# Kernel tuning notes

Measured on AMD Instinct MI355X. Metric: run time of the kernel, lower is better.

The kernel has to match this reference:

```python
import jax, jax.numpy as jnp
import numpy as np

N_NODES = 50000
N_EDGES = 1600000
F_IN = 33
F_OUT = 128
HEADS = 2


def _add_self_loops(row, col, n):
    loop = jnp.arange(n, dtype=row.dtype)
    return jnp.concatenate([row, loop]), jnp.concatenate([col, loop])


def gcn_conv(x, row, col, w, W, b):
    # PyG GCNConv with edge_weight: add self-loops (weight 1), symmetric norm.
    n = x.shape[0]
    row, col = _add_self_loops(row, col, n)
    w = jnp.concatenate([w, jnp.ones((n,), x.dtype)])
    deg = jax.ops.segment_sum(w, col, num_segments=n)
    dinv = jnp.where(deg > 0, jax.lax.rsqrt(deg), 0.0)
    norm = dinv[row] * w * dinv[col]            # [E+N]
    xl = x @ W                                   # [N, F_OUT]
    out = jax.ops.segment_sum(norm[:, None] * xl[row], col, num_segments=n)
    return out + b


def gat_conv(x, row, col, W, att_src, att_dst, b):
    # PyG GATConv, heads=2, concat=False, eval-mode (no attention dropout).
    n = x.shape[0]
    row, col = _add_self_loops(row, col, n)
    xl = (x @ W).reshape(n, HEADS, F_OUT)        # [N, H, C]
    a_src = (xl * att_src).sum(-1)               # [N, H]
    a_dst = (xl * att_dst).sum(-1)               # [N, H]
    e = jax.nn.leaky_relu(a_src[row] + a_dst[col], 0.2)  # [E+N, H]
    m = jax.ops.segment_max(e, col, num_segments=n)      # per-dst max (stable)
    e = jnp.exp(e - m[col])
    s = jax.ops.segment_sum(e, col, num_segments=n)
    alpha = e / s[col]                           # edge softmax per dst node
    out = jax.ops.segment_sum(alpha[:, :, None] * xl[row], col, num_segments=n)
    return out.mean(axis=1) + b                  # concat=False -> head mean


def setup_inputs() -> dict:
    key = jax.random.key(0)
    ks = jax.random.split(key, 16)
    s_in = 1.0 / np.sqrt(F_IN)
    s_h = 1.0 / np.sqrt(F_OUT)
    inp = {
        "target_x": jax.random.normal(ks[0], (N_NODES, F_IN), jnp.float32),
        "target_edge_index": jax.random.randint(ks[1], (2, N_EDGES), 0, N_NODES, jnp.int32),
        "target_weight": jax.random.uniform(ks[2], (N_EDGES,), jnp.float32),
        "gcn_W": jax.random.normal(ks[3], (F_IN, F_OUT), jnp.float32) * s_in,
        "gcn_b": jnp.zeros((F_OUT,), jnp.float32),
        "gat1_W": jax.random.normal(ks[4], (F_OUT, HEADS * F_OUT), jnp.float32) * s_h,
        "gat1_as": jax.random.normal(ks[5], (HEADS, F_OUT), jnp.float32) * s_h,
        "gat1_ad": jax.random.normal(ks[6], (HEADS, F_OUT), jnp.float32) * s_h,
        "gat1_b": jnp.zeros((F_OUT,), jnp.float32),
        "gat2_W": jax.random.normal(ks[7], (F_OUT, HEADS * F_OUT), jnp.float32) * s_h,
        "gat2_as": jax.random.normal(ks[8], (HEADS, F_OUT), jnp.float32) * s_h,
        "gat2_ad": jax.random.normal(ks[9], (HEADS, F_OUT), jnp.float32) * s_h,
        "gat2_b": jnp.zeros((F_OUT,), jnp.float32),
        "fc1_W": jax.random.normal(ks[10], (F_OUT, F_OUT), jnp.float32) * s_h,
        "fc1_b": jnp.zeros((F_OUT,), jnp.float32),
        "fc2_W": jax.random.normal(ks[11], (F_OUT, F_OUT), jnp.float32) * s_h,
        "fc2_b": jnp.zeros((F_OUT,), jnp.float32),
        "pro_bias": jax.random.uniform(ks[12], (1, F_OUT), jnp.float32, -0.2, 0.2),
    }
    return inp


def _forward(target_x, target_weight, gcn_W, gcn_b, gat1_W, gat1_as, gat1_ad,
             gat1_b, gat2_W, gat2_as, gat2_ad, gat2_b, fc1_W, fc1_b,
             fc2_W, fc2_b, pro_bias, row, col):
    # layer 0: GCN + ReLU
    x = jax.nn.relu(gcn_conv(target_x, row, col, target_weight, gcn_W, gcn_b))
    # layer 1: GAT + ReLU, then sigmoid-gated blend
    xt = jax.nn.relu(gat_conv(x, row, col, gat1_W, gat1_as, gat1_ad, gat1_b))
    z = jax.nn.sigmoid(xt @ fc1_W + fc1_b + x @ fc2_W + fc2_b + pro_bias)
    x = z * xt + (1.0 - z) * x
    # layer 2: GAT (no ReLU on last layer), gated blend
    xt = gat_conv(x, row, col, gat2_W, gat2_as, gat2_ad, gat2_b)
    z = jax.nn.sigmoid(xt @ fc1_W + fc1_b + x @ fc2_W + fc2_b + pro_bias)
    return z * xt + (1.0 - z) * x


def reference(target_x, target_edge_index, target_weight, gcn_W, gcn_b,
              gat1_W, gat1_as, gat1_ad, gat1_b, gat2_W, gat2_as, gat2_ad,
              gat2_b, fc1_W, fc1_b, fc2_W, fc2_b, pro_bias):
    row, col = target_edge_index[0], target_edge_index[1]
    return _forward(target_x, target_weight, gcn_W, gcn_b, gat1_W, gat1_as,
                    gat1_ad, gat1_b, gat2_W, gat2_as, gat2_ad, gat2_b,
                    fc1_W, fc1_b, fc2_W, fc2_b, pro_bias, row, col)
```

## Files before the change

### kernel.cpp

```cpp
#include <hip/hip_runtime.h>

#define F_IN 33
#define FP 36
#define C 128
#define GROWS 16
#define MAXDEG 128

__device__ __forceinline__ unsigned short f2bf(float f) {
  unsigned u = __float_as_uint(f);
  unsigned r = (u + 0x7fff + ((u >> 16) & 1)) >> 16;
  return (unsigned short)r;
}
__device__ __forceinline__ unsigned pack2(float lo, float hi) {
  return (unsigned)f2bf(lo) | ((unsigned)f2bf(hi) << 16);
}
__device__ __forceinline__ float bflo(unsigned u) { return __uint_as_float(u << 16); }
__device__ __forceinline__ float bfhi(unsigned u) { return __uint_as_float(u & 0xffff0000u); }


__global__ void count_kernel(const int* __restrict__ col, const float* __restrict__ w,
                             int* __restrict__ cnt, float* __restrict__ deg, int E) {
  int e = blockIdx.x * blockDim.x + threadIdx.x;
  if (e < E) {
    int c = col[e];
    atomicAdd(&cnt[c], 1);
    atomicAdd(&deg[c], w[e]);
  }
}

__global__ void scan1_kernel(const int* __restrict__ cnt, int* __restrict__ out,
                             int* __restrict__ bsum, int n) {
  __shared__ int lds[256];
  int t = threadIdx.x;
  int base = blockIdx.x * 1024 + t * 4;
  int v0 = (base + 0 < n) ? cnt[base + 0] : 0;
  int v1 = (base + 1 < n) ? cnt[base + 1] : 0;
  int v2 = (base + 2 < n) ? cnt[base + 2] : 0;
  int v3 = (base + 3 < n) ? cnt[base + 3] : 0;
  int tot = v0 + v1 + v2 + v3;
  lds[t] = tot;
  __syncthreads();
  for (int o = 1; o < 256; o <<= 1) {
    int x = (t >= o) ? lds[t - o] : 0;
    __syncthreads();
    lds[t] += x;
    __syncthreads();
  }
  int excl = lds[t] - tot;
  if (t == 255) bsum[blockIdx.x] = lds[255];
  if (base + 0 < n) out[base + 0] = excl;
  if (base + 1 < n) out[base + 1] = excl + v0;
  if (base + 2 < n) out[base + 2] = excl + v0 + v1;
  if (base + 3 < n) out[base + 3] = excl + v0 + v1 + v2;
}

__global__ void scan2_kernel(int* __restrict__ bsum, int nb) {
  __shared__ int lds[256];
  int t = threadIdx.x;
  int v = (t < nb) ? bsum[t] : 0;
  lds[t] = v;
  __syncthreads();
  for (int o = 1; o < 256; o <<= 1) {
    int x = (t >= o) ? lds[t - o] : 0;
    __syncthreads();
    lds[t] += x;
    __syncthreads();
  }
  if (t < nb) bsum[t] = lds[t] - v;
}

__global__ void scan3_dinv_kernel(int* __restrict__ off, const int* __restrict__ bsum,
                                  const float* __restrict__ deg, float* __restrict__ dinv,
                                  int n, int N) {
  int i = blockIdx.x * blockDim.x + threadIdx.x;
  if (i < n) off[i] += bsum[i >> 10];
  if (i < N) dinv[i] = rsqrtf(deg[i] + 1.0f);
}

__global__ void scatter_kernel(const int* __restrict__ row, const int* __restrict__ col,
                               const float* __restrict__ w, const int* __restrict__ off,
                               const float* __restrict__ dinv, int* __restrict__ cur,
                               int2* __restrict__ sedge, int E) {
  int e = blockIdx.x * blockDim.x + threadIdx.x;
  if (e < E) {
    int c = col[e];
    int r = row[e];
    int p = off[c] + atomicAdd(&cur[c], 1);
    sedge[p] = make_int2(r, __float_as_int(dinv[r] * w[e]));
  }
}


__global__ void prep_dots_kernel(const float* __restrict__ W1, const float* __restrict__ as1,
                                 const float* __restrict__ ad1, const float* __restrict__ W2,
                                 const float* __restrict__ as2, const float* __restrict__ ad2,
                                 float* __restrict__ attv) {
  int t = blockIdx.x * 256 + threadIdx.x;
  if (t >= 1024) return;
  int layer = t >> 9, rem = t & 511, sd = rem >> 8, rem2 = rem & 255;
  int h = rem2 >> 7, k = rem2 & 127;
  const float* W = layer ? W2 : W1;
  const float* att = sd ? (layer ? ad2 : ad1) : (layer ? as2 : as1);
  float s = 0.f;
  for (int c2 = 0; c2 < C; c2++) s += W[k * 2 * C + h * C + c2] * att[h * C + c2];
  attv[t] = s;
}

__global__ void prep_repack_kernel(const float* __restrict__ W1, const float* __restrict__ W2,
                                   float* __restrict__ Wp1, float* __restrict__ Wp2) {
  int t = blockIdx.x * 256 + threadIdx.x;
  int layer = t >> 15, rem = t & 32767, hk = rem >> 7, j = rem & 127;
  int h = hk >> 7, k = hk & 127;
  const float* W = layer ? W2 : W1;
  float* Wp = layer ? Wp2 : Wp1;
  Wp[hk * C + j] = W[k * 2 * C + h * C + j];
}

__global__ void prep_wz_kernel(const float* __restrict__ fc1W, const float* __restrict__ fc2W,
                               float* __restrict__ Wz) {
  int t = blockIdx.x * 256 + threadIdx.x;
  if (t >= 32768) return;
  Wz[t] = (t < 16384) ? fc1W[t] : fc2W[t - 16384];
}

__global__ void convert_x_kernel(const float* __restrict__ x, unsigned* __restrict__ X36U, int N) {
  int t = blockIdx.x * blockDim.x + threadIdx.x;
  if (t >= N * (FP / 2)) return;
  int n = t / (FP / 2);
  int p = t - n * (FP / 2);
  int c0 = 2 * p, c1 = 2 * p + 1;
  float f0 = (c0 < F_IN) ? x[n * F_IN + c0] : 0.f;
  float f1 = (c1 < F_IN) ? x[n * F_IN + c1] : 0.f;
  X36U[t] = pack2(f0, f1);
}


__global__ __launch_bounds__(256) void gcn_agg33_kernel(
    const unsigned* __restrict__ X36U, const int* __restrict__ off,
    const int2* __restrict__ sedge, const float* __restrict__ dinv,
    float* __restrict__ Xagg, int N) {
  int c = blockIdx.x * 4 + (threadIdx.x >> 6);
  if (c >= N) return;
  int l = threadIdx.x & 63;
  bool act = l < FP / 2;
  float dc = dinv[c];
  unsigned uc = act ? X36U[(unsigned)c * (FP / 2) + l] : 0u;
  float A0x = dc * bflo(uc), A0y = dc * bfhi(uc);
  float A1x = 0.f, A1y = 0.f, A2x = 0.f, A2y = 0.f, A3x = 0.f, A3y = 0.f;
  int p = off[c], p1 = off[c + 1];
  for (; p + 4 <= p1; p += 4) {
    int2 e0 = sedge[p + 0], e1 = sedge[p + 1], e2 = sedge[p + 2], e3 = sedge[p + 3];
    unsigned u0 = 0, u1 = 0, u2 = 0, u3 = 0;
    if (act) {
      u0 = X36U[(unsigned)e0.x * (FP / 2) + l];
      u1 = X36U[(unsigned)e1.x * (FP / 2) + l];
      u2 = X36U[(unsigned)e2.x * (FP / 2) + l];
      u3 = X36U[(unsigned)e3.x * (FP / 2) + l];
    }
    float w0 = __int_as_float(e0.y), w1 = __int_as_float(e1.y);
    float w2 = __int_as_float(e2.y), w3 = __int_as_float(e3.y);
    A0x += w0 * bflo(u0); A0y += w0 * bfhi(u0);
    A1x += w1 * bflo(u1); A1y += w1 * bfhi(u1);
    A2x += w2 * bflo(u2); A2y += w2 * bfhi(u2);
    A3x += w3 * bflo(u3); A3y += w3 * bfhi(u3);
  }
  for (; p < p1; p++) {
    int2 e0 = sedge[p];
    unsigned u0 = act ? X36U[(unsigned)e0.x * (FP / 2) + l] : 0u;
    float w0 = __int_as_float(e0.y);
    A0x += w0 * bflo(u0); A0y += w0 * bfhi(u0);
  }
  if (act) {
    float2 o;
    o.x = dc * (A0x + A1x + A2x + A3x);
    o.y = dc * (A0y + A1y + A2y + A3y);
    ((float2*)Xagg)[(unsigned)c * (FP / 2) + l] = o;
  }
}

__global__ void gemm36_kernel(const float* __restrict__ Xagg, const float* __restrict__ W,
                              const float* __restrict__ b, const float* __restrict__ wsv,
                              const float* __restrict__ wdv, float* __restrict__ H,
                              unsigned short* __restrict__ Hb, float* __restrict__ asrc,
                              float* __restrict__ adst, int N) {
  int n0 = blockIdx.x * GROWS;
  int j = threadIdx.x;
  __shared__ float xr[GROWS * FP];
  __shared__ float xls[GROWS * 132];
  {
    const float4* src = (const float4*)(Xagg + (size_t)n0 * FP);
    float4* dst = (float4*)xr;
    for (int i = j; i < GROWS * FP / 4; i += 128) dst[i] = src[i];
  }
  __syncthreads();
  float acc[GROWS];
  #pragma unroll
  for (int r = 0; r < GROWS; r++) acc[r] = 0.f;
  #pragma unroll 3
  for (int k = 0; k < F_IN; k++) {
    float wv = W[k * C + j];
    #pragma unroll
    for (int r = 0; r < GROWS; r++) acc[r] += xr[r * FP + k] * wv;
  }
  #pragma unroll
  for (int r = 0; r < GROWS; r++) {
    int n = n0 + r;
    float v = fmaxf(acc[r] + b[j], 0.f);
    if (n < N) {
      H[(size_t)n * C + j] = v;
      Hb[(size_t)n * C + j] = f2bf(v);
    }
    xls[r * 132 + j] = v;
  }
  __syncthreads();
  int r = j >> 3, sub = j & 7;
  float sa0 = 0.f, sd0 = 0.f, sa1 = 0.f, sd1 = 0.f;
  for (int k = sub; k < C; k += 8) {
    float v = xls[r * 132 + k];
    sa0 += v * wsv[k];      sd0 += v * wdv[k];
    sa1 += v * wsv[C + k];  sd1 += v * wdv[C + k];
  }
  #pragma unroll
  for (int o = 4; o > 0; o >>= 1) {
    sa0 += __shfl_down(sa0, o); sd0 += __shfl_down(sd0, o);
    sa1 += __shfl_down(sa1, o); sd1 += __shfl_down(sd1, o);
  }
  int n = n0 + r;
  if (sub == 0 && n < N) {
    asrc[n * 2 + 0] = sa0; adst[n * 2 + 0] = sd0;
    asrc[n * 2 + 1] = sa1; adst[n * 2 + 1] = sd1;
  }
}

__global__ __launch_bounds__(256) void gat_agg_kernel(
    const unsigned* __restrict__ HbU, const float* __restrict__ asrc,
    const float* __restrict__ adst, const int* __restrict__ off,
    const int2* __restrict__ sedge, unsigned* __restrict__ AggU, int N) {
  __shared__ float2 lsc[4][MAXDEG];
  int slot = threadIdx.x >> 6;
  int c = blockIdx.x * 4 + slot;
  if (c >= N) return;
  int l = threadIdx.x & 63;
  float2 adc = ((const float2*)adst)[c];
  float2 asc = ((const float2*)asrc)[c];
  int p0 = off[c], p1 = off[c + 1];
  int deg = p1 - p0;
  float e00 = asc.x + adc.x; e00 = e00 > 0.f ? e00 : 0.2f * e00;
  float e01 = asc.y + adc.y; e01 = e01 > 0.f ? e01 : 0.2f * e01;
  float m0 = e00, m1 = e01;
  for (int p = p0 + l; p < p1; p += 64) {
    int r = sedge[p].x;
    float2 av = ((const float2*)asrc)[r];
    float e0 = av.x + adc.x; e0 = e0 > 0.f ? e0 : 0.2f * e0;
    float e1 = av.y + adc.y; e1 = e1 > 0.f ? e1 : 0.2f * e1;
    int i = p - p0;
    if (i < MAXDEG) lsc[slot][i] = make_float2(e0, e1);
    m0 = fmaxf(m0, e0); m1 = fmaxf(m1, e1);
  }
  #pragma unroll
  for (int o = 32; o > 0; o >>= 1) {
    m0 = fmaxf(m0, __shfl_xor(m0, o));
    m1 = fmaxf(m1, __shfl_xor(m1, o));
  }
  int nl = deg < MAXDEG ? deg : MAXDEG;
  float s0 = 0.f, s1 = 0.f;
  for (int i = l; i < nl; i += 64) {
    float2 sc = lsc[slot][i];
    float a0 = __expf(sc.x - m0), a1 = __expf(sc.y - m1);
    lsc[slot][i] = make_float2(a0, a1);
    s0 += a0; s1 += a1;
  }
  for (int p = p0 + MAXDEG + l; p < p1; p += 64) {
    int r = sedge[p].x;
    float2 av = ((const float2*)asrc)[r];
    float e0 = av.x + adc.x; e0 = e0 > 0.f ? e0 : 0.2f * e0;
    float e1 = av.y + adc.y; e1 = e1 > 0.f ? e1 : 0.2f * e1;
    s0 += __expf(e0 - m0); s1 += __expf(e1 - m1);
  }
  #pragma unroll
  for (int o = 32; o > 0; o >>= 1) { s0 += __shfl_xor(s0, o); s1 += __shfl_xor(s1, o); }
  float w0 = __expf(e00 - m0), w1 = __expf(e01 - m1);
  s0 += w0; s1 += w1;
  float inv0 = 1.f / s0, inv1 = 1.f / s1;
  unsigned uc = HbU[(unsigned)c * 64 + l];
  float a00 = w0 * bflo(uc), a01 = w0 * bfhi(uc);
  float a10 = w1 * bflo(uc), a11 = w1 * bfhi(uc);
  float b00 = 0.f, b01 = 0.f, b10 = 0.f, b11 = 0.f;
  int i = 0;
  for (; i + 8 <= nl; i += 8) {
    int r0 = sedge[p0 + i + 0].x, r1 = sedge[p0 + i + 1].x;
    int r2 = sedge[p0 + i + 2].x, r3 = sedge[p0 + i + 3].x;
    int r4 = sedge[p0 + i + 4].x, r5 = sedge[p0 + i + 5].x;
    int r6 = sedge[p0 + i + 6].x, r7 = sedge[p0 + i + 7].x;
    unsigned u0 = HbU[(unsigned)r0 * 64 + l];
    unsigned u1 = HbU[(unsigned)r1 * 64 + l];
    unsigned u2 = HbU[(unsigned)r2 * 64 + l];
    unsigned u3 = HbU[(unsigned)r3 * 64 + l];
    unsigned u4 = HbU[(unsigned)r4 * 64 + l];
    unsigned u5 = HbU[(unsigned)r5 * 64 + l];
    unsigned u6 = HbU[(unsigned)r6 * 64 + l];
    unsigned u7 = HbU[(unsigned)r7 * 64 + l];
    float2 f0 = lsc[slot][i + 0], f1 = lsc[slot][i + 1];
    float2 f2 = lsc[slot][i + 2], f3 = lsc[slot][i + 3];
    float2 f4 = lsc[slot][i + 4], f5 = lsc[slot][i + 5];
    float2 f6 = lsc[slot][i + 6], f7 = lsc[slot][i + 7];
    a00 += f0.x * bflo(u0); a01 += f0.x * bfhi(u0); a10 += f0.y * bflo(u0); a11 += f0.y * bfhi(u0);
    b00 += f1.x * bflo(u1); b01 += f1.x * bfhi(u1); b10 += f1.y * bflo(u1); b11 += f1.y * bfhi(u1);
    a00 += f2.x * bflo(u2); a01 += f2.x * bfhi(u2); a10 += f2.y * bflo(u2); a11 += f2.y * bfhi(u2);
    b00 += f3.x * bflo(u3); b01 += f3.x * bfhi(u3); b10 += f3.y * bflo(u3); b11 += f3.y * bfhi(u3);
    a00 += f4.x * bflo(u4); a01 += f4.x * bfhi(u4); a10 += f4.y * bflo(u4); a11 += f4.y * bfhi(u4);
    b00 += f5.x * bflo(u5); b01 += f5.x * bfhi(u5); b10 += f5.y * bflo(u5); b11 += f5.y * bfhi(u5);
    a00 += f6.x * bflo(u6); a01 += f6.x * bfhi(u6); a10 += f6.y * bflo(u6); a11 += f6.y * bfhi(u6);
    b00 += f7.x * bflo(u7); b01 += f7.x * bfhi(u7); b10 += f7.y * bflo(u7); b11 += f7.y * bfhi(u7);
  }
  for (; i < nl; i++) {
    int r0 = sedge[p0 + i].x;
    unsigned u0 = HbU[(unsigned)r0 * 64 + l];
    float2 f0 = lsc[slot][i];
    a00 += f0.x * bflo(u0); a01 += f0.x * bfhi(u0);
    a10 += f0.y * bflo(u0); a11 += f0.y * bfhi(u0);
  }
  for (int p = p0 + MAXDEG; p < p1; p++) {
    int r = sedge[p].x;
    float2 av = ((const float2*)asrc)[r];
    float e0 = av.x + adc.x; e0 = e0 > 0.f ? e0 : 0.2f * e0;
    float e1 = av.y + adc.y; e1 = e1 > 0.f ? e1 : 0.2f * e1;
    float al0 = __expf(e0 - m0), al1 = __expf(e1 - m1);
    unsigned u0 = HbU[(unsigned)r * 64 + l];
    a00 += al0 * bflo(u0); a01 += al0 * bfhi(u0);
    a10 += al1 * bflo(u0); a11 += al1 * bfhi(u0);
  }
  AggU[(unsigned)c * 128 + l]      = pack2((a00 + b00) * inv0, (a01 + b01) * inv0);
  AggU[(unsigned)c * 128 + 64 + l] = pack2((a10 + b10) * inv1, (a11 + b11) * inv1);
}

__global__ __launch_bounds__(128) void post_gemm_kernel(
    const unsigned* __restrict__ AggU, const float* __restrict__ Wp,
    const float* __restrict__ b, float* __restrict__ XT,
    unsigned short* __restrict__ XTb, int relu, int N) {
  __shared__ unsigned az[GROWS][128];
  int n0 = blockIdx.x * GROWS;
  int t = threadIdx.x;
  {
    const uint4* src = (const uint4*)AggU;
    for (int i = t; i < GROWS * 32; i += 128) {
      int r = i >> 5, cch = i & 31;
      int n = n0 + r;
      uint4 v = (n < N) ? src[(size_t)n * 32 + cch] : make_uint4(0u, 0u, 0u, 0u);
      *(uint4*)&az[r][cch * 4] = v;
    }
  }
  __syncthreads();
  int w = t >> 6;
  int l = t & 63;
  float acc0[8], acc1[8];
  #pragma unroll
  for (int r = 0; r < 8; r++) { acc0[r] = 0.f; acc1[r] = 0.f; }
  for (int k8 = 0; k8 < 256; k8 += 8) {
    float wA[8], wB[8];
    #pragma unroll
    for (int q = 0; q < 8; q++) {
      wA[q] = Wp[(k8 + q) * C + l];
      wB[q] = Wp[(k8 + q) * C + l + 64];
    }
    #pragma unroll
    for (int r = 0; r < 8; r++) {
      uint4 u = *(const uint4*)&az[w * 8 + r][k8 >> 1];
      float v0 = bflo(u.x), v1 = bfhi(u.x), v2 = bflo(u.y), v3 = bfhi(u.y);
      float v4 = bflo(u.z), v5 = bfhi(u.z), v6 = bflo(u.w), v7 = bfhi(u.w);
      acc0[r] += v0*wA[0] + v1*wA[1] + v2*wA[2] + v3*wA[3]
               + v4*wA[4] + v5*wA[5] + v6*wA[6] + v7*wA[7];
      acc1[r] += v0*wB[0] + v1*wB[1] + v2*wB[2] + v3*wB[3]
               + v4*wB[4] + v5*wB[5] + v6*wB[6] + v7*wB[7];
    }
  }
  float bA = b[l], bB = b[l + 64];
  #pragma unroll
  for (int r = 0; r < 8; r++) {
    int n = n0 + w * 8 + r;
    if (n < N) {
      float vA = 0.5f * acc0[r] + bA;
      float vB = 0.5f * acc1[r] + bB;
      if (relu) { vA = fmaxf(vA, 0.f); vB = fmaxf(vB, 0.f); }
      XT[(size_t)n * C + l]      = vA;
      XT[(size_t)n * C + l + 64] = vB;
      XTb[(size_t)n * C + l]      = f2bf(vA);
      XTb[(size_t)n * C + l + 64] = f2bf(vB);
    }
  }
}

__global__ __launch_bounds__(128) void blend_kernel(
    const unsigned* __restrict__ XTbU, const unsigned* __restrict__ XbU,
    const float* __restrict__ XTf, const float* __restrict__ Xf,
    const float* __restrict__ Wz, const float* __restrict__ fc1b,
    const float* __restrict__ fc2b, const float* __restrict__ pb,
    float* __restrict__ out, unsigned short* __restrict__ Hb2,
    const float* __restrict__ wsv, const float* __restrict__ wdv,
    float* __restrict__ asrc, float* __restrict__ adst, int dots, int N) {
  __shared__ unsigned az[GROWS][128];
  __shared__ float xls[GROWS * 132];
  int n0 = blockIdx.x * GROWS;
  int t = threadIdx.x;
  {
    const uint4* s1 = (const uint4*)XTbU;
    const uint4* s2 = (const uint4*)XbU;
    for (int i = t; i < GROWS * 32; i += 128) {
      int r = i >> 5, cch = i & 31;
      int n = n0 + r;
      uint4 v;
      if (n < N) v = (cch < 16) ? s1[(size_t)n * 16 + cch] : s2[(size_t)n * 16 + (cch - 16)];
      else v = make_uint4(0u, 0u, 0u, 0u);
      *(uint4*)&az[r][cch * 4] = v;
    }
  }
  __syncthreads();
  int w = t >> 6;
  int l = t & 63;
  float acc0[8], acc1[8];
  #pragma unroll
  for (int r = 0; r < 8; r++) { acc0[r] = 0.f; acc1[r] = 0.f; }
  for (int k8 = 0; k8 < 256; k8 += 8) {
    float wA[8], wB[8];
    #pragma unroll
    for (int q = 0; q < 8; q++) {
      wA[q] = Wz[(k8 + q) * C + l];
      wB[q] = Wz[(k8 + q) * C + l + 64];
    }
    #pragma unroll
    for (int r = 0; r < 8; r++) {
      uint4 u = *(const uint4*)&az[w * 8 + r][k8 >> 1];
      float v0 = bflo(u.x), v1 = bfhi(u.x), v2 = bflo(u.y), v3 = bfhi(u.y);
      float v4 = bflo(u.z), v5 = bfhi(u.z), v6 = bflo(u.w), v7 = bfhi(u.w);
      acc0[r] += v0*wA[0] + v1*wA[1] + v2*wA[2] + v3*wA[3]
               + v4*wA[4] + v5*wA[5] + v6*wA[6] + v7*wA[7];
      acc1[r] += v0*wB[0] + v1*wB[1] + v2*wB[2] + v3*wB[3]
               + v4*wB[4] + v5*wB[5] + v6*wB[6] + v7*wB[7];
    }
  }
  float bbA = fc1b[l] + fc2b[l] + pb[l];
  float bbB = fc1b[l + 64] + fc2b[l + 64] + pb[l + 64];
  #pragma unroll
  for (int r = 0; r < 8; r++) {
    int rr = w * 8 + r;
    int n = n0 + rr;
    if (n < N) {
      float xtA = XTf[(size_t)n * C + l],      xA = Xf[(size_t)n * C + l];
      float xtB = XTf[(size_t)n * C + l + 64], xB = Xf[(size_t)n * C + l + 64];
      float tA = acc0[r] + bbA, tB = acc1[r] + bbB;
      float zA = 1.f / (1.f + __expf(-tA));
      float zB = 1.f / (1.f + __expf(-tB));
      float oA = zA * xtA + (1.f - zA) * xA;
      float oB = zB * xtB + (1.f - zB) * xB;
      out[(size_t)n * C + l]      = oA;
      out[(size_t)n * C + l + 64] = oB;
      if (dots) {
        Hb2[(size_t)n * C + l]      = f2bf(oA);
        Hb2[(size_t)n * C + l + 64] = f2bf(oB);
      }
      xls[rr * 132 + l] = oA;
      xls[rr * 132 + l + 64] = oB;
    } else {
      xls[rr * 132 + l] = 0.f;
      xls[rr * 132 + l + 64] = 0.f;
    }
  }
  if (!dots) return;
  __syncthreads();
  int r = t >> 3, sub = t & 7;
  float sa0 = 0.f, sd0 = 0.f, sa1 = 0.f, sd1 = 0.f;
  for (int k = sub; k < C; k += 8) {
    float v = xls[r * 132 + k];
    sa0 += v * wsv[k];      sd0 += v * wdv[k];
    sa1 += v * wsv[C + k];  sd1 += v * wdv[C + k];
  }
  #pragma unroll
  for (int o = 4; o > 0; o >>= 1) {
    sa0 += __shfl_down(sa0, o); sd0 += __shfl_down(sd0, o);
    sa1 += __shfl_down(sa1, o); sd1 += __shfl_down(sd1, o);
  }
  int n = n0 + r;
  if (sub == 0 && n < N) {
    asrc[n * 2 + 0] = sa0; adst[n * 2 + 0] = sd0;
    asrc[n * 2 + 1] = sa1; adst[n * 2 + 1] = sd1;
  }
}


extern "C" void kernel_launch(void* const* d_in, const int* in_sizes, int n_in,
                              void* d_out, int out_size, void* d_ws, size_t ws_size,
                              hipStream_t stream) {
  const float* x_in  = (const float*)d_in[0];
  const int*   ei    = (const int*)d_in[1];
  const float* ew    = (const float*)d_in[2];
  const float* gcn_W = (const float*)d_in[3];
  const float* gcn_b = (const float*)d_in[4];
  const float* g1_W  = (const float*)d_in[5];
  const float* g1_as = (const float*)d_in[6];
  const float* g1_ad = (const float*)d_in[7];
  const float* g1_b  = (const float*)d_in[8];
  const float* g2_W  = (const float*)d_in[9];
  const float* g2_as = (const float*)d_in[10];
  const float* g2_ad = (const float*)d_in[11];
  const float* g2_b  = (const float*)d_in[12];
  const float* fc1_W = (const float*)d_in[13];
  const float* fc1_b = (const float*)d_in[14];
  const float* fc2_W = (const float*)d_in[15];
  const float* fc2_b = (const float*)d_in[16];
  const float* pb    = (const float*)d_in[17];

  const int N = in_sizes[0] / F_IN;
  const int E = in_sizes[2];
  const int* row = ei;
  const int* col = ei + E;

  char* ws = (char*)d_ws;
  size_t o = 0;
  auto alloc = [&](size_t bytes) -> void* {
    void* p = ws + o;
    o += (bytes + 255) & ~(size_t)255;
    return p;
  };
  int*   cnt   = (int*)alloc((size_t)(N + 1) * 4);
  int*   cur   = (int*)alloc((size_t)N * 4);
  float* deg   = (float*)alloc((size_t)N * 4);
  size_t zero_bytes = o;
  int*   off   = (int*)alloc((size_t)(N + 1) * 4);
  float* dinv  = (float*)alloc((size_t)N * 4);
  int*   bsum  = (int*)alloc(256 * 4);
  int2*  sedge = (int2*)alloc((size_t)E * 8);
  float* attv  = (float*)alloc(1024 * 4);
  float* Wp1   = (float*)alloc((size_t)256 * C * 4);
  float* Wp2   = (float*)alloc((size_t)256 * C * 4);
  float* Wz    = (float*)alloc((size_t)256 * C * 4);
  float* asrc  = (float*)alloc((size_t)N * 2 * 4);
  float* adst  = (float*)alloc((size_t)N * 2 * 4);
  unsigned* X36U = (unsigned*)alloc((size_t)N * (FP / 2) * 4);
  float* Xagg  = (float*)alloc((size_t)N * FP * 4);
  float* H     = (float*)alloc((size_t)N * C * 4);
  unsigned short* Hb  = (unsigned short*)alloc((size_t)N * C * 2);
  unsigned* AggU = (unsigned*)alloc((size_t)N * 128 * 4);
  float* XT    = (float*)alloc((size_t)N * C * 4);
  unsigned short* XTb = (unsigned short*)alloc((size_t)N * C * 2);
  float* H2    = (float*)alloc((size_t)N * C * 4);
  unsigned short* Hb2 = (unsigned short*)alloc((size_t)N * C * 2);
  (void)ws_size; (void)n_in; (void)out_size;

  float* ws1 = attv + 0,   *wd1 = attv + 256;
  float* ws2 = attv + 512, *wd2 = attv + 768;

  hipMemsetAsync(d_ws, 0, zero_bytes, stream);

  const int tb = 256;
  const int nP = N + 1;
  const int nb = (nP + 1023) / 1024;

  prep_dots_kernel<<<4, 256, 0, stream>>>(g1_W, g1_as, g1_ad, g2_W, g2_as, g2_ad, attv);
  prep_repack_kernel<<<256, 256, 0, stream>>>(g1_W, g2_W, Wp1, Wp2);
  prep_wz_kernel<<<128, 256, 0, stream>>>(fc1_W, fc2_W, Wz);
  convert_x_kernel<<<(N * (FP / 2) + tb - 1) / tb, tb, 0, stream>>>(x_in, X36U, N);

  count_kernel<<<(E + tb - 1) / tb, tb, 0, stream>>>(col, ew, cnt, deg, E);
  scan1_kernel<<<nb, 256, 0, stream>>>(cnt, off, bsum, nP);
  scan2_kernel<<<1, 256, 0, stream>>>(bsum, nb);
  scan3_dinv_kernel<<<(nP + tb - 1) / tb, tb, 0, stream>>>(off, bsum, deg, dinv, nP, N);
  scatter_kernel<<<(E + tb - 1) / tb, tb, 0, stream>>>(row, col, ew, off, dinv, cur, sedge, E);

  gcn_agg33_kernel<<<(N + 3) / 4, 256, 0, stream>>>(X36U, off, sedge, dinv, Xagg, N);
  gemm36_kernel<<<(N + GROWS - 1) / GROWS, C, 0, stream>>>(Xagg, gcn_W, gcn_b, ws1, wd1,
                                                           H, Hb, asrc, adst, N);

  gat_agg_kernel<<<(N + 3) / 4, 256, 0, stream>>>((const unsigned*)Hb, asrc, adst, off, sedge, AggU, N);
  post_gemm_kernel<<<(N + GROWS - 1) / GROWS, C, 0, stream>>>(AggU, Wp1, g1_b, XT, XTb, 1, N);
  blend_kernel<<<(N + GROWS - 1) / GROWS, C, 0, stream>>>(
      (const unsigned*)XTb, (const unsigned*)Hb, XT, H, Wz, fc1_b, fc2_b, pb,
      H2, Hb2, ws2, wd2, asrc, adst, 1, N);

  gat_agg_kernel<<<(N + 3) / 4, 256, 0, stream>>>((const unsigned*)Hb2, asrc, adst, off, sedge, AggU, N);
  post_gemm_kernel<<<(N + GROWS - 1) / GROWS, C, 0, stream>>>(AggU, Wp2, g2_b, XT, XTb, 0, N);
  blend_kernel<<<(N + GROWS - 1) / GROWS, C, 0, stream>>>(
      (const unsigned*)XTb, (const unsigned*)Hb2, XT, H2, Wz, fc1_b, fc2_b, pb,
      (float*)d_out, (unsigned short*)0, ws2, wd2, asrc, adst, 0, N);
}
```

Measured before the change: 1.009 ms.

## Split GAT aggregation into attention kernel plus feature-sliced gather passes

The fused GAT aggregation is split in two. An attention kernel writes per-edge softmax numerators to a global buffer (the output array is reused as scratch), plus per-node self weights and sums. Four gather passes then each handle a 16-column slice of the bf16 features, with lanes spread over edges, aiming to shrink the gathered working set per pass and improve cache hit rate. The GCN degree is now computed from the sorted CSR instead of float atomics, and dinv[row] is applied at gather time; the cost is re-reading edges and alpha four times and extra launches.

```diff
diff --git a/kernel.cpp b/kernel.cpp
--- a/kernel.cpp
+++ b/kernel.cpp
@@ -4,7 +4,6 @@
 #define FP 36
 #define C 128
 #define GROWS 16
-#define MAXDEG 128
 
 __device__ __forceinline__ unsigned short f2bf(float f) {
   unsigned u = __float_as_uint(f);
@@ -18,14 +17,9 @@
 __device__ __forceinline__ float bfhi(unsigned u) { return __uint_as_float(u & 0xffff0000u); }
 
 
-__global__ void count_kernel(const int* __restrict__ col, const float* __restrict__ w,
-                             int* __restrict__ cnt, float* __restrict__ deg, int E) {
+__global__ void count_kernel(const int* __restrict__ col, int* __restrict__ cnt, int E) {
   int e = blockIdx.x * blockDim.x + threadIdx.x;
-  if (e < E) {
-    int c = col[e];
-    atomicAdd(&cnt[c], 1);
-    atomicAdd(&deg[c], w[e]);
-  }
+  if (e < E) atomicAdd(&cnt[col[e]], 1);
 }
 
 __global__ void scan1_kernel(const int* __restrict__ cnt, int* __restrict__ out,
@@ -69,25 +63,34 @@
   if (t < nb) bsum[t] = lds[t] - v;
 }
 
-__global__ void scan3_dinv_kernel(int* __restrict__ off, const int* __restrict__ bsum,
-                                  const float* __restrict__ deg, float* __restrict__ dinv,
-                                  int n, int N) {
+__global__ void scan3_kernel(int* __restrict__ off, const int* __restrict__ bsum, int n) {
   int i = blockIdx.x * blockDim.x + threadIdx.x;
   if (i < n) off[i] += bsum[i >> 10];
-  if (i < N) dinv[i] = rsqrtf(deg[i] + 1.0f);
 }
 
 __global__ void scatter_kernel(const int* __restrict__ row, const int* __restrict__ col,
                                const float* __restrict__ w, const int* __restrict__ off,
-                               const float* __restrict__ dinv, int* __restrict__ cur,
-                               int2* __restrict__ sedge, int E) {
+                               int* __restrict__ cur, int2* __restrict__ sedge, int E) {
   int e = blockIdx.x * blockDim.x + threadIdx.x;
   if (e < E) {
     int c = col[e];
-    int r = row[e];
     int p = off[c] + atomicAdd(&cur[c], 1);
-    sedge[p] = make_int2(r, __float_as_int(dinv[r] * w[e]));
-  }
+    sedge[p] = make_int2(row[e], __float_as_int(w[e]));
+  }
+}
+
+__global__ __launch_bounds__(256) void deg_dinv_kernel(
+    const int* __restrict__ off, const int2* __restrict__ sedge,
+    float* __restrict__ dinv, int N) {
+  int c = blockIdx.x * 4 + (threadIdx.x >> 6);
+  if (c >= N) return;
+  int l = threadIdx.x & 63;
+  float s = 0.f;
+  int p1 = off[c + 1];
+  for (int p = off[c] + l; p < p1; p += 64) s += __int_as_float(sedge[p].y);
+  #pragma unroll
+  for (int o = 32; o > 0; o >>= 1) s += __shfl_xor(s, o);
+  if (l == 0) dinv[c] = rsqrtf(s + 1.0f);
 }
 
 
@@ -157,8 +160,10 @@
       u2 = X36U[(unsigned)e2.x * (FP / 2) + l];
       u3 = X36U[(unsigned)e3.x * (FP / 2) + l];
     }
-    float w0 = __int_as_float(e0.y), w1 = __int_as_float(e1.y);
-    float w2 = __int_as_float(e2.y), w3 = __int_as_float(e3.y);
+    float w0 = dinv[e0.x] * __int_as_float(e0.y);
+    float w1 = dinv[e1.x] * __int_as_float(e1.y);
+    float w2 = dinv[e2.x] * __int_as_float(e2.y);
+    float w3 = dinv[e3.x] * __int_as_float(e3.y);
     A0x += w0 * bflo(u0); A0y += w0 * bfhi(u0);
     A1x += w1 * bflo(u1); A1y += w1 * bfhi(u1);
     A2x += w2 * bflo(u2); A2y += w2 * bfhi(u2);
@@ -167,7 +172,7 @@
   for (; p < p1; p++) {
     int2 e0 = sedge[p];
     unsigned u0 = act ? X36U[(unsigned)e0.x * (FP / 2) + l] : 0u;
-    float w0 = __int_as_float(e0.y);
+    float w0 = dinv[e0.x] * __int_as_float(e0.y);
     A0x += w0 * bflo(u0); A0y += w0 * bfhi(u0);
   }
   if (act) {
@@ -232,19 +237,17 @@
   }
 }
 
-__global__ __launch_bounds__(256) void gat_agg_kernel(
-    const unsigned* __restrict__ HbU, const float* __restrict__ asrc,
-    const float* __restrict__ adst, const int* __restrict__ off,
-    const int2* __restrict__ sedge, unsigned* __restrict__ AggU, int N) {
-  __shared__ float2 lsc[4][MAXDEG];
-  int slot = threadIdx.x >> 6;
-  int c = blockIdx.x * 4 + slot;
+__global__ __launch_bounds__(256) void att_kernel(
+    const float* __restrict__ asrc, const float* __restrict__ adst,
+    const int* __restrict__ off, const int2* __restrict__ sedge,
+    float2* __restrict__ alphaA, float2* __restrict__ selfwA,
+    float2* __restrict__ sarrA, int N) {
+  int c = blockIdx.x * 4 + (threadIdx.x >> 6);
   if (c >= N) return;
   int l = threadIdx.x & 63;
   float2 adc = ((const float2*)adst)[c];
   float2 asc = ((const float2*)asrc)[c];
   int p0 = off[c], p1 = off[c + 1];
-  int deg = p1 - p0;
   float e00 = asc.x + adc.x; e00 = e00 > 0.f ? e00 : 0.2f * e00;
   float e01 = asc.y + adc.y; e01 = e01 > 0.f ? e01 : 0.2f * e01;
   float m0 = e00, m1 = e01;
@@ -253,8 +256,7 @@
     float2 av = ((const float2*)asrc)[r];
     float e0 = av.x + adc.x; e0 = e0 > 0.f ? e0 : 0.2f * e0;
     float e1 = av.y + adc.y; e1 = e1 > 0.f ? e1 : 0.2f * e1;
-    int i = p - p0;
-    if (i < MAXDEG) lsc[slot][i] = make_float2(e0, e1);
+    alphaA[p] = make_float2(e0, e1);
     m0 = fmaxf(m0, e0); m1 = fmaxf(m1, e1);
   }
   #pragma unroll
@@ -262,76 +264,71 @@
     m0 = fmaxf(m0, __shfl_xor(m0, o));
     m1 = fmaxf(m1, __shfl_xor(m1, o));
   }
-  int nl = deg < MAXDEG ? deg : MAXDEG;
   float s0 = 0.f, s1 = 0.f;
-  for (int i = l; i < nl; i += 64) {
-    float2 sc = lsc[slot][i];
+  for (int p = p0 + l; p < p1; p += 64) {
+    float2 sc = alphaA[p];
     float a0 = __expf(sc.x - m0), a1 = __expf(sc.y - m1);
-    lsc[slot][i] = make_float2(a0, a1);
+    alphaA[p] = make_float2(a0, a1);
     s0 += a0; s1 += a1;
-  }
-  for (int p = p0 + MAXDEG + l; p < p1; p += 64) {
-    int r = sedge[p].x;
-    float2 av = ((const float2*)asrc)[r];
-    float e0 = av.x + adc.x; e0 = e0 > 0.f ? e0 : 0.2f * e0;
-    float e1 = av.y + adc.y; e1 = e1 > 0.f ? e1 : 0.2f * e1;
-    s0 += __expf(e0 - m0); s1 += __expf(e1 - m1);
   }
   #pragma unroll
   for (int o = 32; o > 0; o >>= 1) { s0 += __shfl_xor(s0, o); s1 += __shfl_xor(s1, o); }
   float w0 = __expf(e00 - m0), w1 = __expf(e01 - m1);
-  s0 += w0; s1 += w1;
-  float inv0 = 1.f / s0, inv1 = 1.f / s1;
-  unsigned uc = HbU[(unsigned)c * 64 + l];
-  float a00 = w0 * bflo(uc), a01 = w0 * bfhi(uc);
-  float a10 = w1 * bflo(uc), a11 = w1 * bfhi(uc);
-  float b00 = 0.f, b01 = 0.f, b10 = 0.f, b11 = 0.f;
-  int i = 0;
-  for (; i + 8 <= nl; i += 8) {
-    int r0 = sedge[p0 + i + 0].x, r1 = sedge[p0 + i + 1].x;
-    int r2 = sedge[p0 + i + 2].x, r3 = sedge[p0 + i + 3].x;
-    int r4 = sedge[p0 + i + 4].x, r5 = sedge[p0 + i + 5].x;
-    int r6 = sedge[p0 + i + 6].x, r7 = sedge[p0 + i + 7].x;
-    unsigned u0 = HbU[(unsigned)r0 * 64 + l];
-    unsigned u1 = HbU[(unsigned)r1 * 64 + l];
-    unsigned u2 = HbU[(unsigned)r2 * 64 + l];
-    unsigned u3 = HbU[(unsigned)r3 * 64 + l];
-    unsigned u4 = HbU[(unsigned)r4 * 64 + l];
-    unsigned u5 = HbU[(unsigned)r5 * 64 + l];
-    unsigned u6 = HbU[(unsigned)r6 * 64 + l];
-    unsigned u7 = HbU[(unsigned)r7 * 64 + l];
-    float2 f0 = lsc[slot][i + 0], f1 = lsc[slot][i + 1];
-    float2 f2 = lsc[slot][i + 2], f3 = lsc[slot][i + 3];
-    float2 f4 = lsc[slot][i + 4], f5 = lsc[slot][i + 5];
-    float2 f6 = lsc[slot][i + 6], f7 = lsc[slot][i + 7];
-    a00 += f0.x * bflo(u0); a01 += f0.x * bfhi(u0); a10 += f0.y * bflo(u0); a11 += f0.y * bfhi(u0);
-    b00 += f1.x * bflo(u1); b01 += f1.x * bfhi(u1); b10 += f1.y * bflo(u1); b11 += f1.y * bfhi(u1);
-    a00 += f2.x * bflo(u2); a01 += f2.x * bfhi(u2); a10 += f2.y * bflo(u2); a11 += f2.y * bfhi(u2);
-    b00 += f3.x * bflo(u3); b01 += f3.x * bfhi(u3); b10 += f3.y * bflo(u3); b11 += f3.y * bfhi(u3);
-    a00 += f4.x * bflo(u4); a01 += f4.x * bfhi(u4); a10 += f4.y * bflo(u4); a11 += f4.y * bfhi(u4);
-    b00 += f5.x * bflo(u5); b01 += f5.x * bfhi(u5); b10 += f5.y * bflo(u5); b11 += f5.y * bfhi(u5);
-    a00 += f6.x * bflo(u6); a01 += f6.x * bfhi(u6); a10 += f6.y * bflo(u6); a11 += f6.y * bfhi(u6);
-    b00 += f7.x * bflo(u7); b01 += f7.x * bfhi(u7); b10 += f7.y * bflo(u7); b11 += f7.y * bfhi(u7);
-  }
-  for (; i < nl; i++) {
-    int r0 = sedge[p0 + i].x;
-    unsigned u0 = HbU[(unsigned)r0 * 64 + l];
-    float2 f0 = lsc[slot][i];
-    a00 += f0.x * bflo(u0); a01 += f0.x * bfhi(u0);
-    a10 += f0.y * bflo(u0); a11 += f0.y * bfhi(u0);
-  }
-  for (int p = p0 + MAXDEG; p < p1; p++) {
-    int r = sedge[p].x;
-    float2 av = ((const float2*)asrc)[r];
-    float e0 = av.x + adc.x; e0 = e0 > 0.f ? e0 : 0.2f * e0;
-    float e1 = av.y + adc.y; e1 = e1 > 0.f ? e1 : 0.2f * e1;
-    float al0 = __expf(e0 - m0), al1 = __expf(e1 - m1);
-    unsigned u0 = HbU[(unsigned)r * 64 + l];
-    a00 += al0 * bflo(u0); a01 += al0 * bfhi(u0);
-    a10 += al1 * bflo(u0); a11 += al1 * bfhi(u0);
-  }
-  AggU[(unsigned)c * 128 + l]      = pack2((a00 + b00) * inv0, (a01 + b01) * inv0);
-  AggU[(unsigned)c * 128 + 64 + l] = pack2((a10 + b10) * inv1, (a11 + b11) * inv1);
+  if (l == 0) {
+    selfwA[c] = make_float2(w0, w1);
+    sarrA[c]  = make_float2(s0 + w0, s1 + w1);
+  }
+}
+
+__global__ __launch_bounds__(256) void gat_pass_kernel(
+    const unsigned* __restrict__ HbU, const float2* __restrict__ alphaA,
+    const float2* __restrict__ selfwA, const float2* __restrict__ sarrA,
+    const int* __restrict__ off, const int2* __restrict__ sedge,
+    unsigned* __restrict__ AggU, int pass, int N) {
+  int c = blockIdx.x * 4 + (threadIdx.x >> 6);
+  if (c >= N) return;
+  int l = threadIdx.x & 63;
+  int g = l >> 4, lg = l & 15;
+  int fp = 16 * pass + lg;
+  int p0 = off[c], p1 = off[c + 1];
+  float ax = 0.f, ay = 0.f, az = 0.f, aw = 0.f;
+  float bx = 0.f, by = 0.f, bz = 0.f, bw = 0.f;
+  int p = p0 + g;
+  for (; p + 4 < p1; p += 8) {
+    int r0 = sedge[p].x, r1 = sedge[p + 4].x;
+    float2 al0 = alphaA[p], al1 = alphaA[p + 4];
+    unsigned u0 = HbU[(size_t)r0 * 64 + fp];
+    unsigned u1 = HbU[(size_t)r1 * 64 + fp];
+    float x0 = bflo(u0), y0 = bfhi(u0);
+    float x1 = bflo(u1), y1 = bfhi(u1);
+    ax += al0.x * x0; ay += al0.x * y0; az += al0.y * x0; aw += al0.y * y0;
+    bx += al1.x * x1; by += al1.x * y1; bz += al1.y * x1; bw += al1.y * y1;
+  }
+  for (; p < p1; p += 4) {
+    int r0 = sedge[p].x;
+    float2 al0 = alphaA[p];
+    unsigned u0 = HbU[(size_t)r0 * 64 + fp];
+    float x0 = bflo(u0), y0 = bfhi(u0);
+    ax += al0.x * x0; ay += al0.x * y0; az += al0.y * x0; aw += al0.y * y0;
+  }
+  ax += bx; ay += by; az += bz; aw += bw;
+  if (g == 0) {
+    float2 sw = selfwA[c];
+    unsigned uc = HbU[(size_t)c * 64 + fp];
+    float xc = bflo(uc), yc = bfhi(uc);
+    ax += sw.x * xc; ay += sw.x * yc; az += sw.y * xc; aw += sw.y * yc;
+  }
+  #pragma unroll
+  for (int o = 16; o <= 32; o <<= 1) {
+    ax += __shfl_xor(ax, o); ay += __shfl_xor(ay, o);
+    az += __shfl_xor(az, o); aw += __shfl_xor(aw, o);
+  }
+  if (g == 0) {
+    float2 sr = sarrA[c];
+    float inv0 = 1.f / sr.x, inv1 = 1.f / sr.y;
+    AggU[(size_t)c * 128 + fp]      = pack2(ax * inv0, ay * inv0);
+    AggU[(size_t)c * 128 + 64 + fp] = pack2(az * inv1, aw * inv1);
+  }
 }
 
 __global__ __launch_bounds__(128) void post_gemm_kernel(
@@ -523,7 +520,6 @@
   };
   int*   cnt   = (int*)alloc((size_t)(N + 1) * 4);
   int*   cur   = (int*)alloc((size_t)N * 4);
-  float* deg   = (float*)alloc((size_t)N * 4);
   size_t zero_bytes = o;
   int*   off   = (int*)alloc((size_t)(N + 1) * 4);
   float* dinv  = (float*)alloc((size_t)N * 4);
@@ -535,6 +531,8 @@
   float* Wz    = (float*)alloc((size_t)256 * C * 4);
   float* asrc  = (float*)alloc((size_t)N * 2 * 4);
   float* adst  = (float*)alloc((size_t)N * 2 * 4);
+  float2* selfwA = (float2*)alloc((size_t)N * 8);
+  float2* sarrA  = (float2*)alloc((size_t)N * 8);
   unsigned* X36U = (unsigned*)alloc((size_t)N * (FP / 2) * 4);
   float* Xagg  = (float*)alloc((size_t)N * FP * 4);
   float* H     = (float*)alloc((size_t)N * C * 4);
@@ -544,6 +542,7 @@
   unsigned short* XTb = (unsigned short*)alloc((size_t)N * C * 2);
   float* H2    = (float*)alloc((size_t)N * C * 4);
   unsigned short* Hb2 = (unsigned short*)alloc((size_t)N * C * 2);
+  float2* alphaA = (float2*)d_out;
   (void)ws_size; (void)n_in; (void)out_size;
 
   float* ws1 = attv + 0,   *wd1 = attv + 256;
@@ -554,29 +553,37 @@
   const int tb = 256;
   const int nP = N + 1;
   const int nb = (nP + 1023) / 1024;
+  const int nodeg = (N + 3) / 4;
 
   prep_dots_kernel<<<4, 256, 0, stream>>>(g1_W, g1_as, g1_ad, g2_W, g2_as, g2_ad, attv);
   prep_repack_kernel<<<256, 256, 0, stream>>>(g1_W, g2_W, Wp1, Wp2);
   prep_wz_kernel<<<128, 256, 0, stream>>>(fc1_W, fc2_W, Wz);
   convert_x_kernel<<<(N * (FP / 2) + tb - 1) / tb, tb, 0, stream>>>(x_in, X36U, N);
 
-  count_kernel<<<(E + tb - 1) / tb, tb, 0, stream>>>(col, ew, cnt, deg, E);
+  count_kernel<<<(E + tb - 1) / tb, tb, 0, stream>>>(col, cnt, E);
   scan1_kernel<<<nb, 256, 0, stream>>>(cnt, off, bsum, nP);
   scan2_kernel<<<1, 256, 0, stream>>>(bsum, nb);
-  scan3_dinv_kernel<<<(nP + tb - 1) / tb, tb, 0, stream>>>(off, bsum, deg, dinv, nP, N);
-  scatter_kernel<<<(E + tb - 1) / tb, tb, 0, stream>>>(row, col, ew, off, dinv, cur, sedge, E);
-
-  gcn_agg33_kernel<<<(N + 3) / 4, 256, 0, stream>>>(X36U, off, sedge, dinv, Xagg, N);
+  scan3_kernel<<<(nP + tb - 1) / tb, tb, 0, stream>>>(off, bsum, nP);
+  scatter_kernel<<<(E + tb - 1) / tb, tb, 0, stream>>>(row, col, ew, off, cur, sedge, E);
+  deg_dinv_kernel<<<nodeg, 256, 0, stream>>>(off, sedge, dinv, N);
+
+  gcn_agg33_kernel<<<nodeg, 256, 0, stream>>>(X36U, off, sedge, dinv, Xagg, N);
   gemm36_kernel<<<(N + GROWS - 1) / GROWS, C, 0, stream>>>(Xagg, gcn_W, gcn_b, ws1, wd1,
                                                            H, Hb, asrc, adst, N);
 
-  gat_agg_kernel<<<(N + 3) / 4, 256, 0, stream>>>((const unsigned*)Hb, asrc, adst, off, sedge, AggU, N);
+  att_kernel<<<nodeg, 256, 0, stream>>>(asrc, adst, off, sedge, alphaA, selfwA, sarrA, N);
+  for (int p = 0; p < 4; p++)
+    gat_pass_kernel<<<nodeg, 256, 0, stream>>>((const unsigned*)Hb, alphaA, selfwA, sarrA,
+                                               off, sedge, AggU, p, N);
   post_gemm_kernel<<<(N + GROWS - 1) / GROWS, C, 0, stream>>>(AggU, Wp1, g1_b, XT, XTb, 1, N);
   blend_kernel<<<(N + GROWS - 1) / GROWS, C, 0, stream>>>(
       (const unsigned*)XTb, (const unsigned*)Hb, XT, H, Wz, fc1_b, fc2_b, pb,
       H2, Hb2, ws2, wd2, asrc, adst, 1, N);
 
-  gat_agg_kernel<<<(N + 3) / 4, 256, 0, stream>>>((const unsigned*)Hb2, asrc, adst, off, sedge, AggU, N);
+  att_kernel<<<nodeg, 256, 0, stream>>>(asrc, adst, off, sedge, alphaA, selfwA, sarrA, N);
+  for (int p = 0; p < 4; p++)
+    gat_pass_kernel<<<nodeg, 256, 0, stream>>>((const unsigned*)Hb2, alphaA, selfwA, sarrA,
+                                               off, sedge, AggU, p, N);
   post_gemm_kernel<<<(N + GROWS - 1) / GROWS, C, 0, stream>>>(AggU, Wp2, g2_b, XT, XTb, 0, N);
   blend_kernel<<<(N + GROWS - 1) / GROWS, C, 0, stream>>>(
       (const unsigned*)XTb, (const unsigned*)Hb2, XT, H2, Wz, fc1_b, fc2_b, pb,
```

After: 1.169 ms. 1.16x slower.
